# Optimization experiments

Measured on AMD Instinct MI355X. Metric: run time of the kernel, lower is better.

Reference implementation:

```python
import jax, jax.numpy as jnp
import numpy as np

B, T, I, H, O = 64, 512, 64, 1024, 64
STEPS = 49 - 1  # output_len - 1 decode iterations


def _cell(x_t, h, c, Wih, Whh, b):
    # PyTorch LSTM gate order: i, f, g, o
    gates = x_t @ Wih.T + h @ Whh.T + b  # [B, 4H]
    i, f, g, o = jnp.split(gates, 4, axis=-1)
    i = jax.nn.sigmoid(i)
    f = jax.nn.sigmoid(f)
    g = jnp.tanh(g)
    o = jax.nn.sigmoid(o)
    c2 = f * c + i * g
    h2 = o * jnp.tanh(c2)
    return h2, c2


def setup_inputs() -> dict:
    key = jax.random.key(0)
    ks = jax.random.split(key, 12)
    s = 0.05
    return {
        "x": jax.random.normal(ks[0], (B, T, I), jnp.float32),
        "y0": jax.random.normal(ks[1], (B, I), jnp.float32),
        "Wih_e": jax.random.normal(ks[2], (4 * H, I), jnp.float32) * s,
        "Whh_e": jax.random.normal(ks[3], (4 * H, H), jnp.float32) * s,
        "bih_e": jax.random.normal(ks[4], (4 * H,), jnp.float32) * s,
        "bhh_e": jax.random.normal(ks[5], (4 * H,), jnp.float32) * s,
        "Wih_d": jax.random.normal(ks[6], (4 * H, I), jnp.float32) * s,
        "Whh_d": jax.random.normal(ks[7], (4 * H, H), jnp.float32) * s,
        "bih_d": jax.random.normal(ks[8], (4 * H,), jnp.float32) * s,
        "bhh_d": jax.random.normal(ks[9], (4 * H,), jnp.float32) * s,
        "Wfc": jax.random.normal(ks[10], (O, H), jnp.float32) * s,
        "bfc": jax.random.normal(ks[11], (O,), jnp.float32) * s,
    }


def reference(x, y0, Wih_e, Whh_e, bih_e, bhh_e, Wih_d, Whh_d, bih_d, bhh_d, Wfc, bfc):
    b = x.shape[0]
    h0 = jnp.zeros((b, Whh_e.shape[1]), x.dtype)
    c0 = h0

    # Encoder: scan over time (zero initial hidden, as in initHidden)
    be = bih_e + bhh_e

    def enc_step(carry, x_t):
        h, c = carry
        h, c = _cell(x_t, h, c, Wih_e, Whh_e, be)
        return (h, c), None

    (h, c), _ = jax.lax.scan(enc_step, (h0, c0), jnp.swapaxes(x, 0, 1))

    # Decoder: original loop never updates input_decoder -> constant y0 each step.
    bd = bih_d + bhh_d
    xin = y0 @ Wih_d.T + bd  # precompute constant input projection [B, 4H]

    def dec_step(carry, _):
        hd, cd = carry
        gates = xin + hd @ Whh_d.T
        i, f, g, o = jnp.split(gates, 4, axis=-1)
        i = jax.nn.sigmoid(i)
        f = jax.nn.sigmoid(f)
        g = jnp.tanh(g)
        o = jax.nn.sigmoid(o)
        c2 = f * cd + i * g
        h2 = o * jnp.tanh(c2)
        out = h2 @ Wfc.T + bfc  # [B, O]
        return (h2, c2), out

    _, ys = jax.lax.scan(dec_step, (h, c), None, length=STEPS)  # [STEPS, B, O]
    # torch.concat(total, dim=1): step-major along feature axis
    return jnp.swapaxes(ys, 0, 1).reshape(b, STEPS * ys.shape[-1])
```

## Files before the change

### kernel.cpp

```cpp
#include <hip/hip_runtime.h>
#include <hip/hip_fp16.h>

typedef _Float16 f16;
typedef _Float16 f16x8 __attribute__((ext_vector_type(8)));
typedef float f32x16 __attribute__((ext_vector_type(16)));

#define T_N 512
#define DSTEPS 48
#define TOTSTEPS 560
#define NWG 64

#define OFF_WHHE 0ull
#define SZ_WHH   (4096ull*1024*2)
#define OFF_WHHD (OFF_WHHE + SZ_WHH)
#define OFF_WIHE (OFF_WHHD + SZ_WHH)
#define SZ_WIH   (4096ull*64*2)
#define OFF_WIHD (OFF_WIHE + SZ_WIH)
#define OFF_WFC  (OFF_WIHD + SZ_WIH)
#define SZ_WFC   (64ull*1024*2)
#define OFF_XP   (OFF_WFC + SZ_WFC)
#define SZ_XP    (512ull*4096*2)
#define OFF_Y0   (OFF_XP + SZ_XP)
#define SZ_Y0    (4096ull*2)
#define OFF_BE   (OFF_Y0 + SZ_Y0)
#define OFF_BD   (OFF_BE + 4096ull*4)
#define OFF_FLG  (OFF_BD + 4096ull*4)
#define SZ_FLG   (561ull*256*4)
#define OFF_H    ((OFF_FLG + SZ_FLG + 255ull) & ~255ull)

__global__ void prologue(const float* __restrict__ x, const float* __restrict__ y0,
    const float* __restrict__ wihE, const float* __restrict__ whhE,
    const float* __restrict__ bihE, const float* __restrict__ bhhE,
    const float* __restrict__ wihD, const float* __restrict__ whhD,
    const float* __restrict__ bihD, const float* __restrict__ bhhD,
    const float* __restrict__ wfc, char* __restrict__ ws)
{
  const long long gid = (long long)blockIdx.x * 256 + threadIdx.x;
  const long long gsz = (long long)gridDim.x * 256;
  f16* whhEp = (f16*)(ws + OFF_WHHE);
  f16* whhDp = (f16*)(ws + OFF_WHHD);
  f16* wihEp = (f16*)(ws + OFF_WIHE);
  f16* wihDp = (f16*)(ws + OFF_WIHD);
  f16* wfcp  = (f16*)(ws + OFF_WFC);
  f16* xp    = (f16*)(ws + OFF_XP);
  f16* y0p   = (f16*)(ws + OFF_Y0);
  float* be  = (float*)(ws + OFF_BE);
  float* bd  = (float*)(ws + OFF_BD);

  for (long long idx = gid; idx < 4194304ll; idx += gsz) {
    int j = (int)idx & 7, l = (int)(idx >> 3) & 63, kk = (int)(idx >> 9) & 31;
    int i = (int)(idx >> 14) & 1, ks = (int)(idx >> 15) & 1, w = (int)(idx >> 16);
    int nl = i * 32 + (l & 31);
    int grow = (nl >> 4) * 1024 + w * 16 + (nl & 15);
    int k = ks * 512 + kk * 16 + ((l >> 5) << 3) + j;
    whhEp[idx] = (f16)whhE[(long long)grow * 1024 + k];
    whhDp[idx] = (f16)whhD[(long long)grow * 1024 + k];
  }
  for (long long idx = gid; idx < 262144ll; idx += gsz) {
    int j = (int)idx & 7, l = (int)(idx >> 3) & 63, kx = (int)(idx >> 9) & 1;
    int i = (int)(idx >> 10) & 1, ks = (int)(idx >> 11) & 1, w = (int)(idx >> 12);
    int nl = i * 32 + (l & 31);
    int grow = (nl >> 4) * 1024 + w * 16 + (nl & 15);
    int k = (ks * 2 + kx) * 16 + ((l >> 5) << 3) + j;
    wihEp[idx] = (f16)wihE[grow * 64 + k];
    wihDp[idx] = (f16)wihD[grow * 64 + k];
  }
  for (long long idx = gid; idx < 65536ll; idx += gsz) {
    int j = (int)idx & 7, l = (int)(idx >> 3) & 63, kk = (int)(idx >> 9) & 31;
    int i = (int)(idx >> 14) & 1, ks = (int)(idx >> 15) & 1;
    int o = i * 32 + (l & 31);
    int k = ks * 512 + kk * 16 + ((l >> 5) << 3) + j;
    wfcp[idx] = (f16)wfc[o * 1024 + k];
  }
  for (long long idx = gid; idx < 2097152ll; idx += gsz) {
    int kw = (int)idx & 15, b = (int)(idx >> 4) & 63, kkx = (int)(idx >> 10) & 3, t = (int)(idx >> 12);
    xp[idx] = (f16)x[(long long)b * 32768 + t * 64 + kkx * 16 + kw];
  }
  for (long long idx = gid; idx < 4096ll; idx += gsz) {
    int kw = (int)idx & 15, b = (int)(idx >> 4) & 63, kkx = (int)(idx >> 10) & 3;
    y0p[idx] = (f16)y0[b * 64 + kkx * 16 + kw];
  }
  for (long long idx = gid; idx < 4096ll; idx += gsz) {
    be[idx] = bihE[idx] + bhhE[idx];
    bd[idx] = bihD[idx] + bhhD[idx];
  }
}

__device__ __forceinline__ float sigf(float x) { return 1.0f / (1.0f + __expf(-x)); }
__device__ __forceinline__ float tanhfast(float x) {
  x = fminf(fmaxf(x, -15.f), 15.f);
  float e = __expf(2.0f * x);
  return (e - 1.0f) / (e + 1.0f);
}

#define MFMA(a,b,c) __builtin_amdgcn_mfma_f32_32x32x16_f16((a),(b),(c),0,0,0)

__launch_bounds__(256, 1)
__global__ void lstm_persist(char* __restrict__ ws, float* __restrict__ out,
                             const float* __restrict__ bfc)
{
  const int w    = blockIdx.x;
  const int tid  = threadIdx.x;
  const int lane = tid & 63;
  const int wave = tid >> 6;
  const int wm   = wave & 1;
  const int ks   = wave >> 1;

  const f16* whhEp = (const f16*)(ws + OFF_WHHE) + (size_t)w * 65536;
  const f16* whhDp = (const f16*)(ws + OFF_WHHD) + (size_t)w * 65536;
  const f16* wihEp = (const f16*)(ws + OFF_WIHE) + (size_t)w * 4096;
  const f16* wihDp = (const f16*)(ws + OFF_WIHD) + (size_t)w * 4096;
  const f16* wfcp  = (const f16*)(ws + OFF_WFC);
  const f16* xp    = (const f16*)(ws + OFF_XP);
  const f16* y0p   = (const f16*)(ws + OFF_Y0);
  const float* be  = (const float*)(ws + OFF_BE);
  const float* bd  = (const float*)(ws + OFF_BD);
  unsigned* flags  = (unsigned*)(ws + OFF_FLG);
  f16* hb          = (f16*)(ws + OFF_H);

  __shared__ float lds_g[2][64][66];
  __shared__ float bias_s[2][64];
  __shared__ unsigned seen[2];

  if (tid < 64) {
    int g4 = tid >> 4, u = tid & 15;
    bias_s[0][tid] = be[g4 * 1024 + w * 16 + u];
    bias_s[1][tid] = bd[g4 * 1024 + w * 16 + u];
  }
  if (tid < 2) seen[tid] = 0u;

  const int aoff = (wm * 32 + (lane & 31)) * 16 + (lane >> 5) * 8;
  const int boff = lane * 8;
  const int bsel = tid >> 2;
  const int u0   = (tid & 3) * 4;
  const int n0   = lane & 31;

  f16x8 bf0[32], bf1[32];
#pragma unroll
  for (int kk = 0; kk < 32; ++kk) {
    bf0[kk] = *(const f16x8*)(whhEp + (size_t)ks * 32768 + kk * 512 + boff);
    bf1[kk] = *(const f16x8*)(whhEp + (size_t)ks * 32768 + 16384 + kk * 512 + boff);
  }

  float c0 = 0.f, c1 = 0.f, c2 = 0.f, c3 = 0.f;
  __syncthreads();

#pragma unroll 1
  for (int t = 0; t < TOTSTEPS; ++t) {
    const bool enc = (t < T_N);

    if (t == T_N) {
#pragma unroll
      for (int kk = 0; kk < 32; ++kk) {
        bf0[kk] = *(const f16x8*)(whhDp + (size_t)ks * 32768 + kk * 512 + boff);
        bf1[kk] = *(const f16x8*)(whhDp + (size_t)ks * 32768 + 16384 + kk * 512 + boff);
      }
    }

    const f16* xblk = enc ? (xp + (size_t)t * 4096) : y0p;
    const f16* wihp = enc ? wihEp : wihDp;
    f16x8 xa0 = *(const f16x8*)(xblk + (ks * 2 + 0) * 1024 + aoff);
    f16x8 xa1 = *(const f16x8*)(xblk + (ks * 2 + 1) * 1024 + aoff);
    f16x8 wf0 = *(const f16x8*)(wihp + ((ks * 2 + 0) * 2 + 0) * 512 + boff);
    f16x8 wf1 = *(const f16x8*)(wihp + ((ks * 2 + 0) * 2 + 1) * 512 + boff);
    f16x8 wf2 = *(const f16x8*)(wihp + ((ks * 2 + 1) * 2 + 0) * 512 + boff);
    f16x8 wf3 = *(const f16x8*)(wihp + ((ks * 2 + 1) * 2 + 1) * 512 + boff);

    if (t > 0) {
      if (wave < 2) {
        const unsigned* fp = flags + (size_t)t * 256 + wave * 128 + lane;
        int ok;
        do {
          unsigned v0 = __hip_atomic_load(fp,      __ATOMIC_RELAXED, __HIP_MEMORY_SCOPE_AGENT);
          unsigned v1 = __hip_atomic_load(fp + 64, __ATOMIC_RELAXED, __HIP_MEMORY_SCOPE_AGENT);
          ok = __all((v0 == 1u) & (v1 == 1u));
          if (!ok) __builtin_amdgcn_s_sleep(1);
        } while (!ok);
        __hip_atomic_store(&seen[wave], (unsigned)t, __ATOMIC_RELEASE, __HIP_MEMORY_SCOPE_WORKGROUP);
      } else {
        while (__hip_atomic_load(&seen[wm], __ATOMIC_ACQUIRE, __HIP_MEMORY_SCOPE_WORKGROUP) < (unsigned)t)
          __builtin_amdgcn_s_sleep(1);
      }
      asm volatile("" ::: "memory");
    }

    f16x8 af[32];
    if (t > 0) {
      const f16* hblk = hb + (size_t)(t - 1) * 65536;
#pragma unroll
      for (int kk = 0; kk < 32; ++kk)
        af[kk] = *(const f16x8*)(hblk + (size_t)(ks * 32 + kk) * 1024 + aoff);
    }

    f32x16 acc0, acc1;
#pragma unroll
    for (int i = 0; i < 16; ++i) { acc0[i] = 0.f; acc1[i] = 0.f; }
    acc0 = MFMA(xa0, wf0, acc0); acc0 = MFMA(xa1, wf1, acc0);
    acc1 = MFMA(xa0, wf2, acc1); acc1 = MFMA(xa1, wf3, acc1);

    if (t > 0) {
#pragma unroll
      for (int kk = 0; kk < 32; ++kk) {
        acc0 = MFMA(af[kk], bf0[kk], acc0);
        acc1 = MFMA(af[kk], bf1[kk], acc1);
      }
    }

    {
      const float* bs = enc ? bias_s[0] : bias_s[1];
      const float b0h = 0.5f * bs[n0];
      const float b1h = 0.5f * bs[32 + n0];
#pragma unroll
      for (int i = 0; i < 16; ++i) { acc0[i] += b0h; acc1[i] += b1h; }
    }

    {
      const int mb = wm * 32 + ((lane >> 5) << 2);
#pragma unroll
      for (int r = 0; r < 16; ++r) {
        const int m = mb + (r & 3) + ((r >> 2) << 3);
        lds_g[ks][n0][m]      = acc0[r];
        lds_g[ks][32 + n0][m] = acc1[r];
      }
    }
    __syncthreads();

    union { unsigned long long u64; f16 h4[4]; } hu;
    float cc[4] = {c0, c1, c2, c3};
#pragma unroll
    for (int j = 0; j < 4; ++j) {
      const int u = u0 + j;
      float ig = lds_g[0][u][bsel]      + lds_g[1][u][bsel];
      float fg = lds_g[0][16 + u][bsel] + lds_g[1][16 + u][bsel];
      float gg = lds_g[0][32 + u][bsel] + lds_g[1][32 + u][bsel];
      float og = lds_g[0][48 + u][bsel] + lds_g[1][48 + u][bsel];
      float cn = sigf(fg) * cc[j] + sigf(ig) * tanhfast(gg);
      cc[j] = cn;
      hu.h4[j] = (f16)(sigf(og) * tanhfast(cn));
    }
    c0 = cc[0]; c1 = cc[1]; c2 = cc[2]; c3 = cc[3];

    {
      f16* dst = hb + (size_t)t * 65536 + (size_t)w * 1024 + bsel * 16 + u0;
      unsigned long long addr = (unsigned long long)(size_t)dst;
      asm volatile("global_store_dwordx2 %0, %1, off sc0 sc1" : : "v"(addr), "v"(hu.u64) : "memory");
    }
    asm volatile("s_waitcnt vmcnt(0)" ::: "memory");
    if (lane == 0) {
      unsigned* fa = flags + (size_t)(t + 1) * 256 + wave * 64 + w;
      unsigned long long addr = (unsigned long long)(size_t)fa;
      unsigned one = 1u;
      asm volatile("global_store_dword %0, %1, off sc0 sc1" : : "v"(addr), "v"(one) : "memory");
    }
  }

  if (w < DSTEPS) {
    __syncthreads();
    const int s = T_N + 1 + w;
#pragma unroll
    for (int kk = 0; kk < 32; ++kk) {
      bf0[kk] = *(const f16x8*)(wfcp + (size_t)ks * 32768 + kk * 512 + boff);
      bf1[kk] = *(const f16x8*)(wfcp + (size_t)ks * 32768 + 16384 + kk * 512 + boff);
    }
    if (wave < 2) {
      const unsigned* fp = flags + (size_t)s * 256 + wave * 128 + lane;
      int ok;
      do {
        unsigned v0 = __hip_atomic_load(fp,      __ATOMIC_RELAXED, __HIP_MEMORY_SCOPE_AGENT);
        unsigned v1 = __hip_atomic_load(fp + 64, __ATOMIC_RELAXED, __HIP_MEMORY_SCOPE_AGENT);
        ok = __all((v0 == 1u) & (v1 == 1u));
        if (!ok) __builtin_amdgcn_s_sleep(1);
      } while (!ok);
      __hip_atomic_store(&seen[wave], (unsigned)s, __ATOMIC_RELEASE, __HIP_MEMORY_SCOPE_WORKGROUP);
    } else {
      while (__hip_atomic_load(&seen[wm], __ATOMIC_ACQUIRE, __HIP_MEMORY_SCOPE_WORKGROUP) < (unsigned)s)
        __builtin_amdgcn_s_sleep(1);
    }
    asm volatile("" ::: "memory");

    const f16* hblk = hb + (size_t)(s - 1) * 65536;
    f16x8 af[32];
#pragma unroll
    for (int kk = 0; kk < 32; ++kk)
      af[kk] = *(const f16x8*)(hblk + (size_t)(ks * 32 + kk) * 1024 + aoff);

    f32x16 acc0, acc1;
#pragma unroll
    for (int i = 0; i < 16; ++i) { acc0[i] = 0.f; acc1[i] = 0.f; }
#pragma unroll
    for (int kk = 0; kk < 32; ++kk) {
      acc0 = MFMA(af[kk], bf0[kk], acc0);
      acc1 = MFMA(af[kk], bf1[kk], acc1);
    }
    {
      const int mb = wm * 32 + ((lane >> 5) << 2);
#pragma unroll
      for (int r = 0; r < 16; ++r) {
        const int m = mb + (r & 3) + ((r >> 2) << 3);
        lds_g[ks][n0][m]      = acc0[r];
        lds_g[ks][32 + n0][m] = acc1[r];
      }
    }
    __syncthreads();
    const int f0 = (tid & 3) * 16;
    float* op = out + (size_t)bsel * 3072 + w * 64 + f0;
#pragma unroll
    for (int c4 = 0; c4 < 4; ++c4) {
      float v4[4];
#pragma unroll
      for (int j = 0; j < 4; ++j) {
        const int f = f0 + c4 * 4 + j;
        v4[j] = lds_g[0][f][bsel] + lds_g[1][f][bsel] + bfc[f];
      }
      *(float4*)(op + c4 * 4) = make_float4(v4[0], v4[1], v4[2], v4[3]);
    }
  }
}

extern "C" void kernel_launch(void* const* d_in, const int* in_sizes, int n_in,
                              void* d_out, int out_size, void* d_ws, size_t ws_size,
                              hipStream_t stream) {
  const float* x    = (const float*)d_in[0];
  const float* y0   = (const float*)d_in[1];
  const float* wihE = (const float*)d_in[2];
  const float* whhE = (const float*)d_in[3];
  const float* bihE = (const float*)d_in[4];
  const float* bhhE = (const float*)d_in[5];
  const float* wihD = (const float*)d_in[6];
  const float* whhD = (const float*)d_in[7];
  const float* bihD = (const float*)d_in[8];
  const float* bhhD = (const float*)d_in[9];
  const float* wfc  = (const float*)d_in[10];
  const float* bfc  = (const float*)d_in[11];
  char* ws   = (char*)d_ws;
  float* out = (float*)d_out;

  prologue<<<256, 256, 0, stream>>>(x, y0, wihE, whhE, bihE, bhhE,
                                    wihD, whhD, bihD, bhhD, wfc, ws);
  lstm_persist<<<NWG, 256, 0, stream>>>(ws, out, bfc);
}
```

Measured before the change: 2.776 ms.

## Speculatively load hidden state before flag wait, validate via poison sentinel

The prologue now fills the hidden-state history buffer with a poison bit pattern. Each step issues its hidden-state loads as relaxed atomics before waiting on the flags, then checks the loaded values for poison and reloads if any is present. The vmcnt wait between the h store and the flag store is also removed. The goal is to hide global load latency behind the inter-workgroup barrier, at the cost of a large poison-fill pass in the prologue and weaker ordering between data and flag stores.

After: 9.034 ms. +225.4%, slower.

```diff
diff --git a/kernel.cpp b/kernel.cpp
--- a/kernel.cpp
+++ b/kernel.cpp
@@ -27,6 +27,8 @@
 #define OFF_FLG  (OFF_BD + 4096ull*4)
 #define SZ_FLG   (561ull*256*4)
 #define OFF_H    ((OFF_FLG + SZ_FLG + 255ull) & ~255ull)
+
+#define POISON 0x7FFF7FFFu
 
 __global__ void prologue(const float* __restrict__ x, const float* __restrict__ y0,
     const float* __restrict__ wihE, const float* __restrict__ whhE,
@@ -84,6 +86,12 @@
     be[idx] = bihE[idx] + bhhE[idx];
     bd[idx] = bihD[idx] + bhhD[idx];
   }
+  {
+    uint4* hp4 = (uint4*)(ws + OFF_H);
+    const uint4 pz = make_uint4(POISON, POISON, POISON, POISON);
+    for (long long idx = gid; idx < 4587520ll; idx += gsz)
+      hp4[idx] = pz;
+  }
 }
 
 __device__ __forceinline__ float sigf(float x) { return 1.0f / (1.0f + __expf(-x)); }
@@ -94,6 +102,29 @@
 }
 
 #define MFMA(a,b,c) __builtin_amdgcn_mfma_f32_32x32x16_f16((a),(b),(c),0,0,0)
+
+#define AF_LOAD(hq) do { \
+  _Pragma("unroll") \
+  for (int kk_ = 0; kk_ < 32; ++kk_) { \
+    afu[kk_].q[0] = __hip_atomic_load((hq) + kk_ * 256,     __ATOMIC_RELAXED, __HIP_MEMORY_SCOPE_AGENT); \
+    afu[kk_].q[1] = __hip_atomic_load((hq) + kk_ * 256 + 1, __ATOMIC_RELAXED, __HIP_MEMORY_SCOPE_AGENT); \
+  } \
+} while (0)
+
+#define AF_CHECK_RETRY(hq) do { \
+  while (1) { \
+    unsigned bad_ = 0u; \
+    _Pragma("unroll") \
+    for (int kk_ = 0; kk_ < 32; ++kk_) { \
+      bad_ |= ((unsigned)afu[kk_].q[0] == POISON) | ((unsigned)(afu[kk_].q[0] >> 32) == POISON); \
+      bad_ |= ((unsigned)afu[kk_].q[1] == POISON) | ((unsigned)(afu[kk_].q[1] >> 32) == POISON); \
+    } \
+    if (!__any(bad_)) break; \
+    __builtin_amdgcn_s_sleep(1); \
+    AF_LOAD(hq); \
+  } \
+  asm volatile("" ::: "memory"); \
+} while (0)
 
 __launch_bounds__(256, 1)
 __global__ void lstm_persist(char* __restrict__ ws, float* __restrict__ out,
@@ -142,6 +173,11 @@
     bf1[kk] = *(const f16x8*)(whhEp + (size_t)ks * 32768 + 16384 + kk * 512 + boff);
   }
 
+  const size_t afoff8 = (size_t)(ks * 65536 + aoff * 2) >> 3;
+
+  union AU { unsigned long long q[2]; f16x8 h; };
+  AU afu[32];
+
   float c0 = 0.f, c1 = 0.f, c2 = 0.f, c3 = 0.f;
   __syncthreads();
 
@@ -165,6 +201,13 @@
     f16x8 wf1 = *(const f16x8*)(wihp + ((ks * 2 + 0) * 2 + 1) * 512 + boff);
     f16x8 wf2 = *(const f16x8*)(wihp + ((ks * 2 + 1) * 2 + 0) * 512 + boff);
     f16x8 wf3 = *(const f16x8*)(wihp + ((ks * 2 + 1) * 2 + 1) * 512 + boff);
+
+    const unsigned long long* hq =
+        (const unsigned long long*)(hb + (size_t)(t - 1) * 65536) + afoff8;
+    if (t > 0) {
+      AF_LOAD(hq);
+      asm volatile("" ::: "memory");
+    }
 
     if (t > 0) {
       if (wave < 2) {
@@ -181,15 +224,7 @@
         while (__hip_atomic_load(&seen[wm], __ATOMIC_ACQUIRE, __HIP_MEMORY_SCOPE_WORKGROUP) < (unsigned)t)
           __builtin_amdgcn_s_sleep(1);
       }
-      asm volatile("" ::: "memory");
-    }
-
-    f16x8 af[32];
-    if (t > 0) {
-      const f16* hblk = hb + (size_t)(t - 1) * 65536;
-#pragma unroll
-      for (int kk = 0; kk < 32; ++kk)
-        af[kk] = *(const f16x8*)(hblk + (size_t)(ks * 32 + kk) * 1024 + aoff);
+      AF_CHECK_RETRY(hq);
     }
 
     f32x16 acc0, acc1;
@@ -201,8 +236,8 @@
     if (t > 0) {
 #pragma unroll
       for (int kk = 0; kk < 32; ++kk) {
-        acc0 = MFMA(af[kk], bf0[kk], acc0);
-        acc1 = MFMA(af[kk], bf1[kk], acc1);
+        acc0 = MFMA(afu[kk].h, bf0[kk], acc0);
+        acc1 = MFMA(afu[kk].h, bf1[kk], acc1);
       }
     }
 
@@ -245,7 +280,6 @@
       unsigned long long addr = (unsigned long long)(size_t)dst;
       asm volatile("global_store_dwordx2 %0, %1, off sc0 sc1" : : "v"(addr), "v"(hu.u64) : "memory");
     }
-    asm volatile("s_waitcnt vmcnt(0)" ::: "memory");
     if (lane == 0) {
       unsigned* fa = flags + (size_t)(t + 1) * 256 + wave * 64 + w;
       unsigned long long addr = (unsigned long long)(size_t)fa;
@@ -262,6 +296,10 @@
       bf0[kk] = *(const f16x8*)(wfcp + (size_t)ks * 32768 + kk * 512 + boff);
       bf1[kk] = *(const f16x8*)(wfcp + (size_t)ks * 32768 + 16384 + kk * 512 + boff);
     }
+    const unsigned long long* hq =
+        (const unsigned long long*)(hb + (size_t)(s - 1) * 65536) + afoff8;
+    AF_LOAD(hq);
+    asm volatile("" ::: "memory");
     if (wave < 2) {
       const unsigned* fp = flags + (size_t)s * 256 + wave * 128 + lane;
       int ok;
@@ -276,21 +314,15 @@
       while (__hip_atomic_load(&seen[wm], __ATOMIC_ACQUIRE, __HIP_MEMORY_SCOPE_WORKGROUP) < (unsigned)s)
         __builtin_amdgcn_s_sleep(1);
     }
-    asm volatile("" ::: "memory");
-
-    const f16* hblk = hb + (size_t)(s - 1) * 65536;
-    f16x8 af[32];
-#pragma unroll
-    for (int kk = 0; kk < 32; ++kk)
-      af[kk] = *(const f16x8*)(hblk + (size_t)(ks * 32 + kk) * 1024 + aoff);
+    AF_CHECK_RETRY(hq);
 
     f32x16 acc0, acc1;
 #pragma unroll
     for (int i = 0; i < 16; ++i) { acc0[i] = 0.f; acc1[i] = 0.f; }
 #pragma unroll
     for (int kk = 0; kk < 32; ++kk) {
-      acc0 = MFMA(af[kk], bf0[kk], acc0);
-      acc1 = MFMA(af[kk], bf1[kk], acc1);
+      acc0 = MFMA(afu[kk].h, bf0[kk], acc0);
+      acc1 = MFMA(afu[kk].h, bf1[kk], acc1);
     }
     {
       const int mb = wm * 32 + ((lane >> 5) << 2);
```
